# Kernel optimization log

Hardware: AMD Instinct MI355X
Metric: run time of the kernel (lower is better)

## Reference

```python
import jax, jax.numpy as jnp
import numpy as np

# Quantization constants from the original module
X_SCALE, X_ZP = 0.0215, -25
Y_SCALE, Y_ZP = 0.0176, 18


def setup_inputs() -> dict:
    key = jax.random.key(0)
    kx, ky = jax.random.split(key)
    K, N = 8192, 16384
    # int8 stand-ins (enum lacks int8); values fit int8 range
    x = jax.random.randint(kx, (K,), 0, 127, dtype=jnp.int32)
    y = jax.random.randint(ky, (K, N), 0, 127, dtype=jnp.int32)
    return {"x": x, "y": y}


def reference(x, y):
    # dequantize_per_tensor: (q - zero_point) * scale, in fp32
    xf = (x.astype(jnp.float32) - X_ZP) * X_SCALE   # [K]
    yf = (y.astype(jnp.float32) - Y_ZP) * Y_SCALE   # [K, N]
    # vector-matrix matmul -> [N]
    return xf @ yf
```

## Files before the change

### kernel.cpp

```cpp
#include <hip/hip_runtime.h>


constexpr int K = 8192;
constexpr int N = 16384;
constexpr float X_SCALE = 0.0215f;
constexpr int   X_ZP    = -25;
constexpr float Y_SCALE = 0.0176f;
constexpr int   Y_ZP    = 18;

constexpr int BLOCK = 256;
constexpr int VEC   = 4;
constexpr int COLS_PER_BLOCK = BLOCK * VEC;
constexpr int NBLK_N = N / COLS_PER_BLOCK;
constexpr int SPLIT_K = 128;
constexpr int KCHUNK = K / SPLIT_K;
constexpr int N4 = N / 4;

typedef int ivec4 __attribute__((ext_vector_type(4)));

__global__ __launch_bounds__(BLOCK, 8) void qgemv_partial(const int* __restrict__ x,
                                                          const ivec4* __restrict__ y,
                                                          ivec4* __restrict__ ws) {
    __shared__ int xs[KCHUNK];

    const int nb = blockIdx.x % NBLK_N;
    const int kc = blockIdx.x / NBLK_N;
    const int k0 = kc * KCHUNK;

    if (threadIdx.x < KCHUNK)
        xs[threadIdx.x] = x[k0 + threadIdx.x] - X_ZP;
    __syncthreads();

    const int col4 = nb * (COLS_PER_BLOCK / 4) + threadIdx.x;
    const ivec4* __restrict__ yv = y + (size_t)k0 * N4 + col4;

    const int r0 = (13 * kc + 7 * nb) & (KCHUNK - 1);

    int acc0 = 0, acc1 = 0, acc2 = 0, acc3 = 0;
    int sx = 0;

#pragma unroll 8
    for (int i = 0; i < KCHUNK; ++i) {
        int k = r0 + i;
        if (k >= KCHUNK) k -= KCHUNK;
        ivec4 v = yv[(size_t)k * N4];
        int a = xs[k];
        sx   += a;
        acc0 += a * v.x;
        acc1 += a * v.y;
        acc2 += a * v.z;
        acc3 += a * v.w;
    }

    const int corr = Y_ZP * sx;
    ivec4 p;
    p.x = acc0 - corr;
    p.y = acc1 - corr;
    p.z = acc2 - corr;
    p.w = acc3 - corr;
    ws[(size_t)kc * N4 + col4] = p;
}

constexpr int RBLK = 128;
constexpr int CPB  = N4 / RBLK;
constexpr int GRP  = BLOCK / CPB;
constexpr int PER  = SPLIT_K / GRP;

__global__ __launch_bounds__(BLOCK) void qgemv_reduce(const ivec4* __restrict__ ws,
                                                      float* __restrict__ out) {
    __shared__ ivec4 red[GRP][CPB];
    const int c = threadIdx.x % CPB;
    const int g = threadIdx.x / CPB;
    const int col4 = blockIdx.x * CPB + c;

    int sx = 0, sy = 0, sz = 0, sw = 0;
#pragma unroll
    for (int i = 0; i < PER; ++i) {
        ivec4 v = ws[(size_t)(g * PER + i) * N4 + col4];
        sx += v.x; sy += v.y; sz += v.z; sw += v.w;
    }
    ivec4 p; p.x = sx; p.y = sy; p.z = sz; p.w = sw;
    red[g][c] = p;
    __syncthreads();

    if (g == 0) {
        ivec4 t = red[0][c];
#pragma unroll
        for (int gg = 1; gg < GRP; ++gg) {
            ivec4 v = red[gg][c];
            t.x += v.x; t.y += v.y; t.z += v.z; t.w += v.w;
        }
        const float s = X_SCALE * Y_SCALE;
        float4 o;
        o.x = s * (float)t.x;
        o.y = s * (float)t.y;
        o.z = s * (float)t.z;
        o.w = s * (float)t.w;
        ((float4*)out)[col4] = o;
    }
}

extern "C" void kernel_launch(void* const* d_in, const int* in_sizes, int n_in,
                              void* d_out, int out_size, void* d_ws, size_t ws_size,
                              hipStream_t stream) {
    const int* x = (const int*)d_in[0];
    const ivec4* y = (const ivec4*)d_in[1];
    float* out = (float*)d_out;
    ivec4* ws = (ivec4*)d_ws;

    qgemv_partial<<<SPLIT_K * NBLK_N, BLOCK, 0, stream>>>(x, y, ws);
    qgemv_reduce<<<RBLK, BLOCK, 0, stream>>>(ws, out);
}
```

Baseline: 673.3 us.

## Stream half the y rows through async LDS DMA with double buffering

Reworks the partial-GEMV inner loop to handle four K rows per step. Two of the rows are fetched asynchronously into a per-wave double-buffered LDS region with global_load_lds, one step ahead. The other two are read directly with nontemporal vector loads. The intent is more outstanding memory traffic and less cache pollution on this bandwidth-bound 512 MB stream. It drops the rotated K start offset that spread accesses across channels, and it relies on the compiler inserting the correct waits before the LDS reads.

```diff
diff --git a/kernel.cpp b/kernel.cpp
--- a/kernel.cpp
+++ b/kernel.cpp
@@ -1,4 +1,5 @@
 #include <hip/hip_runtime.h>
+#include <stdint.h>
 
 
 constexpr int K = 8192;
@@ -9,8 +10,7 @@
 constexpr int   Y_ZP    = 18;
 
 constexpr int BLOCK = 256;
-constexpr int VEC   = 4;
-constexpr int COLS_PER_BLOCK = BLOCK * VEC;
+constexpr int COLS_PER_BLOCK = 1024;
 constexpr int NBLK_N = N / COLS_PER_BLOCK;
 constexpr int SPLIT_K = 128;
 constexpr int KCHUNK = K / SPLIT_K;
@@ -18,39 +18,58 @@
 
 typedef int ivec4 __attribute__((ext_vector_type(4)));
 
+#define AS1 __attribute__((address_space(1)))
+#define AS3 __attribute__((address_space(3)))
+
 __global__ __launch_bounds__(BLOCK, 8) void qgemv_partial(const int* __restrict__ x,
-                                                          const ivec4* __restrict__ y,
+                                                          const int* __restrict__ y,
                                                           ivec4* __restrict__ ws) {
     __shared__ int xs[KCHUNK];
+    __shared__ int dbuf[2][2][COLS_PER_BLOCK];
 
+    const int tid = threadIdx.x;
     const int nb = blockIdx.x % NBLK_N;
     const int kc = blockIdx.x / NBLK_N;
     const int k0 = kc * KCHUNK;
 
-    if (threadIdx.x < KCHUNK)
-        xs[threadIdx.x] = x[k0 + threadIdx.x] - X_ZP;
+    if (tid < KCHUNK) xs[tid] = x[k0 + tid] - X_ZP;
     __syncthreads();
 
-    const int col4 = nb * (COLS_PER_BLOCK / 4) + threadIdx.x;
-    const ivec4* __restrict__ yv = y + (size_t)k0 * N4 + col4;
+    const int* yrow = y + (size_t)k0 * N + nb * COLS_PER_BLOCK;
+    const int wq = (tid >> 6) * 256;
 
-    const int r0 = (13 * kc + 7 * nb) & (KCHUNK - 1);
+#define STAGE(r, b, slot)                                                              \
+    __builtin_amdgcn_global_load_lds((const AS1 void*)(yrow + (size_t)(r) * N + tid * 4), \
+                                     (AS3 void*)(&dbuf[b][slot][wq]), 16, 0, 0)
 
     int acc0 = 0, acc1 = 0, acc2 = 0, acc3 = 0;
     int sx = 0;
 
-#pragma unroll 8
-    for (int i = 0; i < KCHUNK; ++i) {
-        int k = r0 + i;
-        if (k >= KCHUNK) k -= KCHUNK;
-        ivec4 v = yv[(size_t)k * N4];
-        int a = xs[k];
-        sx   += a;
-        acc0 += a * v.x;
-        acc1 += a * v.y;
-        acc2 += a * v.z;
-        acc3 += a * v.w;
+    STAGE(0, 0, 0);
+    STAGE(1, 0, 1);
+
+    int b = 0;
+#pragma unroll 4
+    for (int s = 0; s < KCHUNK / 4; ++s) {
+        const int r = 4 * s;
+        if (s + 1 < KCHUNK / 4) {
+            STAGE(r + 4, b ^ 1, 0);
+            STAGE(r + 5, b ^ 1, 1);
+        }
+        ivec4 v2 = __builtin_nontemporal_load((const ivec4*)(yrow + (size_t)(r + 2) * N) + tid);
+        ivec4 v3 = __builtin_nontemporal_load((const ivec4*)(yrow + (size_t)(r + 3) * N) + tid);
+        ivec4 u0 = *(const ivec4*)&dbuf[b][0][tid * 4];
+        ivec4 u1 = *(const ivec4*)&dbuf[b][1][tid * 4];
+
+        const int a0 = xs[r], a1 = xs[r + 1], a2 = xs[r + 2], a3 = xs[r + 3];
+        sx += a0 + a1 + a2 + a3;
+        acc0 += a0 * u0.x + a1 * u1.x + a2 * v2.x + a3 * v3.x;
+        acc1 += a0 * u0.y + a1 * u1.y + a2 * v2.y + a3 * v3.y;
+        acc2 += a0 * u0.z + a1 * u1.z + a2 * v2.z + a3 * v3.z;
+        acc3 += a0 * u0.w + a1 * u1.w + a2 * v2.w + a3 * v3.w;
+        b ^= 1;
     }
+#undef STAGE
 
     const int corr = Y_ZP * sx;
     ivec4 p;
@@ -58,6 +77,7 @@
     p.y = acc1 - corr;
     p.z = acc2 - corr;
     p.w = acc3 - corr;
+    const int col4 = nb * (COLS_PER_BLOCK / 4) + tid;
     ws[(size_t)kc * N4 + col4] = p;
 }
 
@@ -104,7 +124,7 @@
                               void* d_out, int out_size, void* d_ws, size_t ws_size,
                               hipStream_t stream) {
     const int* x = (const int*)d_in[0];
-    const ivec4* y = (const ivec4*)d_in[1];
+    const int* y = (const int*)d_in[1];
     float* out = (float*)d_out;
     ivec4* ws = (ivec4*)d_ws;
 
```

Result: slower. 700.5 us (+4.0%).
